# Kernel optimization log

Measured on AMD Instinct MI355X. Metric: run time of the kernel, lower is better.

## Reference

```python
import jax, jax.numpy as jnp
import numpy as np

H = 1024          # hidden_size
NH = 16           # num_attention_heads
HD = H // NH      # attention_head_size = 64
B, S = 8, 1024
LN_EPS = 1e-12


def setup_inputs() -> dict:
    key = jax.random.key(0)
    ks = jax.random.split(key, 12)
    sc = 0.02
    return {
        "input_tensor": jax.random.normal(ks[0], (B, S, H), dtype=jnp.float32),
        "attention_mask": jnp.zeros((B, S), dtype=jnp.float32),
        # LinearMem params (quantization disabled -> plain Linear, torch layout [out,in])
        "Wq": jax.random.normal(ks[1], (H, H), dtype=jnp.float32) * sc,
        "bq": jnp.zeros((H,), dtype=jnp.float32),
        "Wk": jax.random.normal(ks[2], (H, H), dtype=jnp.float32) * sc,
        "bk": jnp.zeros((H,), dtype=jnp.float32),
        "Wv": jax.random.normal(ks[3], (H, H), dtype=jnp.float32) * sc,
        "bv": jnp.zeros((H,), dtype=jnp.float32),
        "Wo": jax.random.normal(ks[4], (H, H), dtype=jnp.float32) * sc,
        "bo": jnp.zeros((H,), dtype=jnp.float32),
        "ln_gamma": jnp.ones((H,), dtype=jnp.float32),
        "ln_beta": jnp.zeros((H,), dtype=jnp.float32),
    }


def _heads(x):  # [B,S,H] -> [B,NH,S,HD]
    return x.reshape(B, S, NH, HD).transpose(0, 2, 1, 3)


def reference(input_tensor, attention_mask, Wq, bq, Wk, bk, Wv, bv, Wo, bo, ln_gamma, ln_beta):
    # Q/K/V projections (LinearMem with quantization disabled == Linear)
    q = _heads(jnp.einsum('bsh,oh->bso', input_tensor, Wq) + bq)
    k = _heads(jnp.einsum('bsh,oh->bso', input_tensor, Wk) + bk)
    v = _heads(jnp.einsum('bsh,oh->bso', input_tensor, Wv) + bv)
    scores = jnp.einsum('bnqd,bnkd->bnqk', q, k) / np.float32(np.sqrt(HD))
    scores = scores + attention_mask[:, None, None, :]  # additive mask [B,1,1,S]
    probs = jax.nn.softmax(scores, axis=-1)  # dropout = identity in eval
    ctx = jnp.einsum('bnqk,bnkd->bnqd', probs, v)
    ctx = ctx.transpose(0, 2, 1, 3).reshape(B, S, H)
    # output projection + residual LayerNorm (eps=1e-12)
    out = jnp.einsum('bsh,oh->bso', ctx, Wo) + bo
    resid = out + input_tensor
    mu = jnp.mean(resid, axis=-1, keepdims=True)
    var = jnp.mean(jnp.square(resid - mu), axis=-1, keepdims=True)
    return (resid - mu) * jax.lax.rsqrt(var + LN_EPS) * ln_gamma + ln_beta
```

## Files before the change

kernel.cpp:

```cpp
#include <hip/hip_runtime.h>

#define NHh 16

typedef unsigned short ushortT;
typedef __attribute__((ext_vector_type(8))) short short8;
typedef __attribute__((ext_vector_type(4))) float floatx4;

__device__ __forceinline__ ushortT f2bf(float x) {
    union { float f; unsigned int u; } cv; cv.f = x;
    unsigned int u = cv.u;
    unsigned int r = u + 0x7fffu + ((u >> 16) & 1u);
    return (ushortT)(r >> 16);
}

__device__ __forceinline__ unsigned pack2_trunc(float a, float b) {
    union { float f; unsigned u; } ua, ub;
    ua.f = a; ub.f = b;
    return (ub.u & 0xffff0000u) | (ua.u >> 16);
}

__device__ __forceinline__ void gload_lds16(const ushortT* g, ushortT* l) {
    __builtin_amdgcn_global_load_lds(
        (const __attribute__((address_space(1))) void*)g,
        (__attribute__((address_space(3))) void*)l, 16, 0, 0);
}

__global__ __launch_bounds__(256) void cvt_x(const float* __restrict__ in,
                                             ushortT* __restrict__ out, int n4) {
    int i = blockIdx.x * 256 + threadIdx.x;
    if (i >= n4) return;
    float4 f = ((const float4*)in)[i];
    uint2 o;
    o.x = (unsigned)f2bf(f.x) | ((unsigned)f2bf(f.y) << 16);
    o.y = (unsigned)f2bf(f.z) | ((unsigned)f2bf(f.w) << 16);
    ((uint2*)out)[i] = o;
}

__global__ __launch_bounds__(256) void cvt_w(const float* __restrict__ W0, const float* __restrict__ W1,
                                             const float* __restrict__ W2, const float* __restrict__ W3,
                                             ushortT* __restrict__ o0, ushortT* __restrict__ o1,
                                             ushortT* __restrict__ o2, ushortT* __restrict__ o3, int n4) {
    int z = blockIdx.y;
    const float* in = (z == 0) ? W0 : (z == 1) ? W1 : (z == 2) ? W2 : W3;
    ushortT* out = (z == 0) ? o0 : (z == 1) ? o1 : (z == 2) ? o2 : o3;
    int i = blockIdx.x * 256 + threadIdx.x;
    if (i >= n4) return;
    float4 f = ((const float4*)in)[i];
    uint2 o;
    o.x = (unsigned)f2bf(f.x) | ((unsigned)f2bf(f.y) << 16);
    o.y = (unsigned)f2bf(f.z) | ((unsigned)f2bf(f.w) << 16);
    ((uint2*)out)[i] = o;
}

__device__ __forceinline__ void gemm_core_256x128(
        const ushortT* __restrict__ Ap, const ushortT* __restrict__ Bp,
        int arow0, int brow0, ushortT* As3, ushortT* Bs3,
        int tid, int wr, int wc, int qd, int ln, floatx4 (&acc)[4][4]) {
    const ushortT* srcA[4]; const ushortT* srcB[2];
    int oA[4], oB[2];
#pragma unroll
    for (int k = 0; k < 4; k++) {
        int o = k * 8192 + tid * 16;
        int rowblk = o >> 11, ks = (o >> 10) & 1, r = (o >> 6) & 15;
        int c2 = ((o >> 4) & 3) ^ ((r >> 3) << 1);
        srcA[k] = Ap + (size_t)(arow0 + rowblk * 16 + r) * 1024 + ks * 32 + c2 * 8;
        oA[k] = o;
    }
#pragma unroll
    for (int k = 0; k < 2; k++) {
        int o = k * 8192 + tid * 16;
        int rowblk = o >> 11, ks = (o >> 10) & 1, r = (o >> 6) & 15;
        int c2 = ((o >> 4) & 3) ^ ((r >> 3) << 1);
        srcB[k] = Bp + (size_t)(brow0 + rowblk * 16 + r) * 1024 + ks * 32 + c2 * 8;
        oB[k] = o;
    }
#pragma unroll
    for (int t = 0; t < 2; t++) {
#pragma unroll
        for (int k = 0; k < 4; k++) {
            gload_lds16(srcA[k], (ushortT*)((char*)As3 + t * 32768 + oA[k]));
            srcA[k] += 64;
        }
#pragma unroll
        for (int k = 0; k < 2; k++) {
            gload_lds16(srcB[k], (ushortT*)((char*)Bs3 + t * 16384 + oB[k]));
            srcB[k] += 64;
        }
    }
    asm volatile("s_waitcnt vmcnt(6)" ::: "memory");
    __builtin_amdgcn_s_barrier();

    const int lnc = ln * 64 + ((qd ^ ((ln >> 3) << 1)) * 16);

    int bi = 0, si = 2;
    for (int T = 0; T < 16; T++) {
        const char* Ab = (const char*)As3 + bi * 32768;
        const char* Bb = (const char*)Bs3 + bi * 16384;
        short8 afr[4][2], bfr[4][2];
#pragma unroll
        for (int mi = 0; mi < 4; mi++)
#pragma unroll
            for (int ks = 0; ks < 2; ks++)
                afr[mi][ks] = *(const short8*)(Ab + (mi * 4 + wr) * 2048 + ks * 1024 + lnc);
#pragma unroll
        for (int ni = 0; ni < 4; ni++)
#pragma unroll
            for (int ks = 0; ks < 2; ks++)
                bfr[ni][ks] = *(const short8*)(Bb + (ni * 2 + wc) * 2048 + ks * 1024 + lnc);
        if (T < 14) {
#pragma unroll
            for (int k = 0; k < 4; k++) {
                gload_lds16(srcA[k], (ushortT*)((char*)As3 + si * 32768 + oA[k]));
                srcA[k] += 64;
            }
#pragma unroll
            for (int k = 0; k < 2; k++) {
                gload_lds16(srcB[k], (ushortT*)((char*)Bs3 + si * 16384 + oB[k]));
                srcB[k] += 64;
            }
        }
        __builtin_amdgcn_s_barrier();
        asm volatile("s_waitcnt lgkmcnt(0)" ::: "memory");
        __builtin_amdgcn_sched_barrier(0);
        __builtin_amdgcn_s_setprio(1);
#pragma unroll
        for (int mi = 0; mi < 4; mi++)
#pragma unroll
            for (int ni = 0; ni < 4; ni++)
#pragma unroll
                for (int ks = 0; ks < 2; ks++)
                    acc[mi][ni] = __builtin_amdgcn_mfma_f32_16x16x32_bf16(
                        afr[mi][ks], bfr[ni][ks], acc[mi][ni], 0, 0, 0);
        __builtin_amdgcn_s_setprio(0);
        if (T < 14) { asm volatile("s_waitcnt vmcnt(6)" ::: "memory"); }
        else        { asm volatile("s_waitcnt vmcnt(0)" ::: "memory"); }
        __builtin_amdgcn_s_barrier();
        bi = (bi == 2) ? 0 : bi + 1;
        si = (si == 2) ? 0 : si + 1;
    }
}

__global__ __launch_bounds__(512, 1) void qkv_gemm3(
        const ushortT* __restrict__ X,
        const ushortT* __restrict__ W0, const ushortT* __restrict__ W1, const ushortT* __restrict__ W2,
        const float* __restrict__ b0, const float* __restrict__ b1, const float* __restrict__ b2,
        ushortT* __restrict__ Qo, ushortT* __restrict__ Ko, ushortT* __restrict__ Vo) {
    __shared__ __align__(16) ushortT As3[3 * 16384];
    __shared__ __align__(16) ushortT Bs3[3 * 8192];

    const int l = blockIdx.x;
    const int xcd = l & 7;
    const int j = l >> 3;
    const int tid = threadIdx.x;
    const int lane = tid & 63;
    const int w = tid >> 6;
    const int wr = w >> 1, wc = w & 1;
    const int qd = lane >> 4, ln = lane & 15;

    int z, arow0, brow0;
    const ushortT* Ap; const ushortT* Bp;
    if (j < 64) {
        z = j >> 5;
        int mg = (j >> 3) & 3;
        int n = j & 7;
        arow0 = (mg * 8 + xcd) * 256;
        brow0 = n * 128;
        Ap = X; Bp = z ? W1 : W0;
    } else {
        z = 2;
        int j2 = j - 64;
        arow0 = (j2 & 3) * 256;
        brow0 = ((j2 >> 2) * 8 + xcd) * 128;
        Ap = W2; Bp = X;
    }

    floatx4 acc[4][4];
#pragma unroll
    for (int i = 0; i < 4; i++)
#pragma unroll
        for (int jj = 0; jj < 4; jj++) acc[i][jj] = (floatx4){0.f, 0.f, 0.f, 0.f};

    gemm_core_256x128(Ap, Bp, arow0, brow0, As3, Bs3, tid, wr, wc, qd, ln, acc);

    if (z == 2) {
        floatx4 bv4[4];
#pragma unroll
        for (int mi = 0; mi < 4; mi++)
            bv4[mi] = *(const floatx4*)(b2 + arow0 + mi * 64 + wr * 16 + qd * 4);
#pragma unroll
        for (int ni = 0; ni < 4; ni++) {
            int n = brow0 + ni * 32 + wc * 16 + ln;
            int bb = n >> 10, s = n & 1023;
#pragma unroll
            for (int mi = 0; mi < 4; mi++) {
#pragma unroll
                for (int r2 = 0; r2 < 4; r2++) {
                    int dim = arow0 + mi * 64 + wr * 16 + qd * 4 + r2;
                    int hh = dim >> 6, dd = dim & 63;
                    Vo[((size_t)(bb * NHh + hh) * 64 + dd) * 1024 + s] =
                        f2bf(acc[mi][ni][r2] + bv4[mi][r2]);
                }
            }
        }
    } else {
        ushortT* Out = z ? Ko : Qo;
        const float* bias = z ? b1 : b0;
#pragma unroll
        for (int ni = 0; ni < 4; ni++) {
            int n = brow0 + ni * 32 + wc * 16 + ln;
            float bb = bias[n];
            int h = n >> 6, d = n & 63;
#pragma unroll
            for (int mi = 0; mi < 4; mi++) {
#pragma unroll
                for (int r2 = 0; r2 < 4; r2++) {
                    int m = arow0 + mi * 64 + wr * 16 + qd * 4 + r2;
                    int b = m >> 10, s = m & 1023;
                    Out[(size_t)((b * NHh + h) * 1024 + s) * 64 + d] =
                        f2bf(acc[mi][ni][r2] + bb);
                }
            }
        }
    }
}

__global__ __launch_bounds__(512, 1) void oproj_gemm3(const ushortT* __restrict__ A,
        const ushortT* __restrict__ Wt, const float* __restrict__ bias, float* __restrict__ Pj) {
    __shared__ __align__(16) ushortT As3[3 * 16384];
    __shared__ __align__(16) ushortT Bs3[3 * 8192];

    const int l = blockIdx.x;
    const int xcd = l & 7;
    const int j = l >> 3;
    const int tid = threadIdx.x;
    const int lane = tid & 63;
    const int w = tid >> 6;
    const int wr = w >> 1, wc = w & 1;
    const int qd = lane >> 4, ln = lane & 15;

    const int arow0 = ((j & 3) * 8 + xcd) * 256;
    const int brow0 = (j >> 2) * 128;

    floatx4 acc[4][4];
#pragma unroll
    for (int i = 0; i < 4; i++)
#pragma unroll
        for (int jj = 0; jj < 4; jj++) acc[i][jj] = (floatx4){0.f, 0.f, 0.f, 0.f};

    gemm_core_256x128(A, Wt, arow0, brow0, As3, Bs3, tid, wr, wc, qd, ln, acc);

#pragma unroll
    for (int ni = 0; ni < 4; ni++) {
        int n = brow0 + ni * 32 + wc * 16 + ln;
        float bb = bias[n];
#pragma unroll
        for (int mi = 0; mi < 4; mi++) {
#pragma unroll
            for (int r2 = 0; r2 < 4; r2++) {
                int m = arow0 + mi * 64 + wr * 16 + qd * 4 + r2;
                Pj[(size_t)m * 1024 + n] = acc[mi][ni][r2] + bb;
            }
        }
    }
}

__global__ __launch_bounds__(256, 2) void attn_kernel(const ushortT* __restrict__ Q,
        const ushortT* __restrict__ K, const ushortT* __restrict__ Vg_t,
        const float* __restrict__ mask, ushortT* __restrict__ ctx) {
    __shared__ __align__(16) ushortT Ks[128 * 64];
    __shared__ __align__(16) ushortT Vt[64 * 128];
    __shared__ __align__(16) ushortT Ps[4][64 * 72];

    const int tid = threadIdx.x;
    const int lane = tid & 63;
    const int w = tid >> 6;
    const int qd = lane >> 4;
    const int ln = lane & 15;
    const int l = blockIdx.x;
    const int bh = l & 127;
    const int b = bh >> 4;
    const int h = bh & 15;
    const int qb = l >> 7;

    const ushortT* Qg = Q + (size_t)bh * 65536;
    const ushortT* Kg = K + (size_t)bh * 65536;
    const ushortT* Vg = Vg_t + (size_t)bh * 65536;
    const float* mrow = mask + b * 1024;
    const float LOG2E = 1.4426950408889634f;
    const float SCL = 0.125f * 1.4426950408889634f;

    short8 qf[4][2];
#pragma unroll
    for (int nj = 0; nj < 4; nj++)
#pragma unroll
        for (int ks = 0; ks < 2; ks++)
            qf[nj][ks] = *(const short8*)(Qg + (size_t)(qb * 256 + w * 64 + nj * 16 + ln) * 64 + ks * 32 + qd * 8);

    float lst[4] = {0.f, 0.f, 0.f, 0.f};
    floatx4 accO[4][4];
#pragma unroll
    for (int i = 0; i < 4; i++)
#pragma unroll
        for (int j = 0; j < 4; j++) accO[i][j] = (floatx4){0.f, 0.f, 0.f, 0.f};

    const int ksr = lane >> 3;
    const int kc  = lane & 7;
    const int vdr = lane >> 4;
    const int vcc = lane & 15;

    for (int kt = 0; kt < 8; ++kt) {
        __syncthreads();

#pragma unroll
        for (int ii = 0; ii < 4; ii++) {
            int i = w * 4 + ii;
            int srow = i * 8 + ksr;
            gload_lds16(Kg + (size_t)(kt * 128 + srow) * 64 + (kc ^ ksr) * 8,
                        Ks + i * 512 + lane * 8);
        }
#pragma unroll
        for (int ii = 0; ii < 4; ii++) {
            int i = w * 4 + ii;
            int d = i * 4 + vdr;
            gload_lds16(Vg + (size_t)d * 1024 + kt * 128 + (vcc ^ (d & 15)) * 8,
                        Vt + i * 512 + lane * 8);
        }

        __syncthreads();

#pragma unroll
        for (int h2 = 0; h2 < 2; ++h2) {
            const int s0g = kt * 128 + h2 * 64;

#pragma unroll
            for (int njp = 0; njp < 2; ++njp) {
                floatx4 sv[4][2];
#pragma unroll
                for (int mi = 0; mi < 4; mi++)
#pragma unroll
                    for (int j = 0; j < 2; j++) sv[mi][j] = (floatx4){0.f, 0.f, 0.f, 0.f};
#pragma unroll
                for (int ks = 0; ks < 2; ks++) {
                    short8 af[4];
#pragma unroll
                    for (int mi = 0; mi < 4; mi++)
                        af[mi] = *(const short8*)&Ks[(h2 * 64 + mi * 16 + ln) * 64 +
                                                     (((ks * 4 + qd) ^ (ln & 7)) * 8)];
#pragma unroll
                    for (int mi = 0; mi < 4; mi++)
#pragma unroll
                        for (int j = 0; j < 2; j++)
                            sv[mi][j] = __builtin_amdgcn_mfma_f32_16x16x32_bf16(af[mi], qf[njp * 2 + j][ks], sv[mi][j], 0, 0, 0);
                }

                float rs0 = 0.f, rs1 = 0.f;
#pragma unroll
                for (int mi = 0; mi < 4; mi++) {
                    floatx4 m4 = *(const floatx4*)(mrow + s0g + mi * 16 + qd * 4);
                    float p00 = __builtin_amdgcn_exp2f(sv[mi][0][0] * SCL + m4[0] * LOG2E);
                    float p01 = __builtin_amdgcn_exp2f(sv[mi][0][1] * SCL + m4[1] * LOG2E);
                    float p02 = __builtin_amdgcn_exp2f(sv[mi][0][2] * SCL + m4[2] * LOG2E);
                    float p03 = __builtin_amdgcn_exp2f(sv[mi][0][3] * SCL + m4[3] * LOG2E);
                    float p10 = __builtin_amdgcn_exp2f(sv[mi][1][0] * SCL + m4[0] * LOG2E);
                    float p11 = __builtin_amdgcn_exp2f(sv[mi][1][1] * SCL + m4[1] * LOG2E);
                    float p12 = __builtin_amdgcn_exp2f(sv[mi][1][2] * SCL + m4[2] * LOG2E);
                    float p13 = __builtin_amdgcn_exp2f(sv[mi][1][3] * SCL + m4[3] * LOG2E);
                    rs0 += (p00 + p01) + (p02 + p03);
                    rs1 += (p10 + p11) + (p12 + p13);
                    uint2 w0, w1;
                    w0.x = pack2_trunc(p00, p01); w0.y = pack2_trunc(p02, p03);
                    w1.x = pack2_trunc(p10, p11); w1.y = pack2_trunc(p12, p13);
                    *(uint2*)&Ps[w][(njp * 32 + ln) * 72 + mi * 16 + qd * 4] = w0;
                    *(uint2*)&Ps[w][(njp * 32 + 16 + ln) * 72 + mi * 16 + qd * 4] = w1;
                }
                rs0 += __shfl_xor(rs0, 16, 64); rs0 += __shfl_xor(rs0, 32, 64);
                rs1 += __shfl_xor(rs1, 16, 64); rs1 += __shfl_xor(rs1, 32, 64);
                lst[njp * 2 + 0] += rs0;
                lst[njp * 2 + 1] += rs1;
            }

#pragma unroll
            for (int ks2 = 0; ks2 < 2; ks2++) {
                short8 ap[4], bv[4];
#pragma unroll
                for (int i = 0; i < 4; i++)
                    ap[i] = *(const short8*)&Ps[w][(i * 16 + ln) * 72 + ks2 * 32 + qd * 8];
#pragma unroll
                for (int j = 0; j < 4; j++)
                    bv[j] = *(const short8*)&Vt[(j * 16 + ln) * 128 +
                                                (((h2 * 8 + ks2 * 4 + qd) ^ ln) * 8)];
#pragma unroll
                for (int i = 0; i < 4; i++)
#pragma unroll
                    for (int j = 0; j < 4; j++)
                        accO[i][j] = __builtin_amdgcn_mfma_f32_16x16x32_bf16(ap[i], bv[j], accO[i][j], 0, 0, 0);
            }
        }
    }

#pragma unroll
    for (int i = 0; i < 4; i++) {
#pragma unroll
        for (int r = 0; r < 4; r++) {
            float lv = __shfl(lst[i], qd * 4 + r, 64);
            float linv = 1.f / lv;
            int q = qb * 256 + w * 64 + i * 16 + qd * 4 + r;
#pragma unroll
            for (int j = 0; j < 4; j++) {
                int d = j * 16 + ln;
                ctx[((size_t)(b * 1024 + q)) * 1024 + h * 64 + d] = f2bf(accO[i][j][r] * linv);
            }
        }
    }
}

__global__ __launch_bounds__(256) void ln_kernel(const float* __restrict__ Pj, const float* __restrict__ X,
        const float* __restrict__ gamma, const float* __restrict__ beta, float* __restrict__ out) {
    __shared__ float red[8];
    int row = blockIdx.x;
    int t = threadIdx.x;
    const float4 p4 = ((const float4*)(Pj + (size_t)row * 1024))[t];
    const float4 x4 = ((const float4*)(X + (size_t)row * 1024))[t];
    float r0 = p4.x + x4.x, r1 = p4.y + x4.y, r2 = p4.z + x4.z, r3 = p4.w + x4.w;
    float s = r0 + r1 + r2 + r3;
    float ss = r0 * r0 + r1 * r1 + r2 * r2 + r3 * r3;
#pragma unroll
    for (int o = 1; o < 64; o <<= 1) { s += __shfl_xor(s, o, 64); ss += __shfl_xor(ss, o, 64); }
    int w = t >> 6;
    if ((t & 63) == 0) { red[w] = s; red[4 + w] = ss; }
    __syncthreads();
    s = red[0] + red[1] + red[2] + red[3];
    ss = red[4] + red[5] + red[6] + red[7];
    float mu = s * (1.f / 1024.f);
    float var = ss * (1.f / 1024.f) - mu * mu;
    float inv = rsqrtf(var + 1e-12f);
    const float4 g4 = ((const float4*)gamma)[t];
    const float4 b4 = ((const float4*)beta)[t];
    float4 o4;
    o4.x = (r0 - mu) * inv * g4.x + b4.x;
    o4.y = (r1 - mu) * inv * g4.y + b4.y;
    o4.z = (r2 - mu) * inv * g4.z + b4.z;
    o4.w = (r3 - mu) * inv * g4.w + b4.w;
    ((float4*)(out + (size_t)row * 1024))[t] = o4;
}

extern "C" void kernel_launch(void* const* d_in, const int* in_sizes, int n_in,
                              void* d_out, int out_size, void* d_ws, size_t ws_size,
                              hipStream_t stream) {
    const float* x     = (const float*)d_in[0];
    const float* mask  = (const float*)d_in[1];
    const float* Wq    = (const float*)d_in[2];
    const float* bq    = (const float*)d_in[3];
    const float* Wk    = (const float*)d_in[4];
    const float* bk    = (const float*)d_in[5];
    const float* Wv    = (const float*)d_in[6];
    const float* bv    = (const float*)d_in[7];
    const float* Wo    = (const float*)d_in[8];
    const float* bo    = (const float*)d_in[9];
    const float* gamma = (const float*)d_in[10];
    const float* beta  = (const float*)d_in[11];
    float* out = (float*)d_out;

    char* ws = (char*)d_ws;
    ushortT* Xb  = (ushortT*)(ws);
    ushortT* Wqb = (ushortT*)(ws + (16u << 20));
    ushortT* Wkb = (ushortT*)(ws + (18u << 20));
    ushortT* Wvb = (ushortT*)(ws + (20u << 20));
    ushortT* Wob = (ushortT*)(ws + (22u << 20));
    ushortT* Qb  = (ushortT*)(ws + (24u << 20));
    ushortT* Kb  = (ushortT*)(ws + (40u << 20));
    ushortT* Vb  = (ushortT*)(ws + (56u << 20));
    ushortT* Cb  = (ushortT*)(ws);
    float*   Pj  = (float*)(ws + (24u << 20));

    cvt_x<<<8192, 256, 0, stream>>>(x, Xb, 2097152);
    cvt_w<<<dim3(1024, 4), 256, 0, stream>>>(Wq, Wk, Wv, Wo, Wqb, Wkb, Wvb, Wob, 262144);
    qkv_gemm3<<<768, 512, 0, stream>>>(Xb, Wqb, Wkb, Wvb, bq, bk, bv, Qb, Kb, Vb);
    attn_kernel<<<512, 256, 0, stream>>>(Qb, Kb, Vb, mask, Cb);
    oproj_gemm3<<<256, 512, 0, stream>>>(Cb, Wob, bo, Pj);
    ln_kernel<<<8192, 256, 0, stream>>>(Pj, x, gamma, beta, out);
}
```

Before: 289.0 us.

## Replace QKV GEMM with fused 256x192 tile kernel over concatenated weights

The Q, K and V weights are now converted into one contiguous [3072,1024] bf16 buffer. A new qkv_st kernel computes 256x192 output tiles over this concatenated N dimension, using 512 blocks instead of 768 and a double-buffered LDS pipeline instead of the triple-buffered shared core. V is no longer computed transposed (W2 x X). It is written from the normal orientation with packed ushort4 stores along the sequence dimension. The aim is fewer, larger tiles with better A reuse. The cost is a shallower prefetch pipeline (vmcnt(0) every iteration), higher register pressure from 24 accumulators per wave, and uneven waves when 512 blocks run on 256 CUs.

```diff
diff --git a/kernel.cpp b/kernel.cpp
--- a/kernel.cpp
+++ b/kernel.cpp
@@ -38,11 +38,10 @@
 
 __global__ __launch_bounds__(256) void cvt_w(const float* __restrict__ W0, const float* __restrict__ W1,
                                              const float* __restrict__ W2, const float* __restrict__ W3,
-                                             ushortT* __restrict__ o0, ushortT* __restrict__ o1,
-                                             ushortT* __restrict__ o2, ushortT* __restrict__ o3, int n4) {
+                                             ushortT* __restrict__ Wall, ushortT* __restrict__ Wob, int n4) {
     int z = blockIdx.y;
     const float* in = (z == 0) ? W0 : (z == 1) ? W1 : (z == 2) ? W2 : W3;
-    ushortT* out = (z == 0) ? o0 : (z == 1) ? o1 : (z == 2) ? o2 : o3;
+    ushortT* out = (z < 3) ? (Wall + (size_t)z * 1048576) : Wob;
     int i = blockIdx.x * 256 + threadIdx.x;
     if (i >= n4) return;
     float4 f = ((const float4*)in)[i];
@@ -50,6 +49,137 @@
     o.x = (unsigned)f2bf(f.x) | ((unsigned)f2bf(f.y) << 16);
     o.y = (unsigned)f2bf(f.z) | ((unsigned)f2bf(f.w) << 16);
     ((uint2*)out)[i] = o;
+}
+
+__global__ __launch_bounds__(512, 1) void qkv_st(
+        const ushortT* __restrict__ X, const ushortT* __restrict__ Wall,
+        const float* __restrict__ b0, const float* __restrict__ b1, const float* __restrict__ b2,
+        ushortT* __restrict__ Qo, ushortT* __restrict__ Ko, ushortT* __restrict__ Vo) {
+    __shared__ __align__(16) ushortT As[2 * 16384];
+    __shared__ __align__(16) ushortT Bs[2 * 12288];
+
+    const int l = blockIdx.x;
+    const int xcd = l & 7;
+    const int j = l >> 3;
+    const int mg = j >> 4;
+    const int nt = j & 15;
+    const int arow0 = (mg * 8 + xcd) * 256;
+    const int brow0 = nt * 192;
+
+    const int tid = threadIdx.x;
+    const int lane = tid & 63;
+    const int w = tid >> 6;
+    const int wr = w >> 2;
+    const int wc = w & 3;
+    const int qd = lane >> 4, ln = lane & 15;
+
+    const ushortT* srcA[4]; const ushortT* srcB[3];
+    int oA[4], oB[3];
+#pragma unroll
+    for (int k = 0; k < 4; k++) {
+        int o = k * 8192 + tid * 16;
+        int rowblk = o >> 11, ks = (o >> 10) & 1, r = (o >> 6) & 15;
+        int c2 = ((o >> 4) & 3) ^ ((r >> 3) << 1);
+        srcA[k] = X + (size_t)(arow0 + rowblk * 16 + r) * 1024 + ks * 32 + c2 * 8;
+        oA[k] = o;
+    }
+#pragma unroll
+    for (int k = 0; k < 3; k++) {
+        int o = k * 8192 + tid * 16;
+        int rowblk = o >> 11, ks = (o >> 10) & 1, r = (o >> 6) & 15;
+        int c2 = ((o >> 4) & 3) ^ ((r >> 3) << 1);
+        srcB[k] = Wall + (size_t)(brow0 + rowblk * 16 + r) * 1024 + ks * 32 + c2 * 8;
+        oB[k] = o;
+    }
+
+    floatx4 acc[8][3];
+#pragma unroll
+    for (int i = 0; i < 8; i++)
+#pragma unroll
+        for (int jj = 0; jj < 3; jj++) acc[i][jj] = (floatx4){0.f, 0.f, 0.f, 0.f};
+
+#pragma unroll
+    for (int k = 0; k < 4; k++) { gload_lds16(srcA[k], As + oA[k] / 2); srcA[k] += 64; }
+#pragma unroll
+    for (int k = 0; k < 3; k++) { gload_lds16(srcB[k], Bs + oB[k] / 2); srcB[k] += 64; }
+    asm volatile("s_waitcnt vmcnt(0)" ::: "memory");
+    __builtin_amdgcn_s_barrier();
+
+    const int lnc = ln * 64 + ((qd ^ ((ln >> 3) << 1)) * 16);
+
+    for (int T = 0; T < 16; T++) {
+        const char* Ab = (const char*)As + (T & 1) * 32768;
+        const char* Bb = (const char*)Bs + (T & 1) * 24576;
+        short8 afr[8][2], bfr[3][2];
+#pragma unroll
+        for (int mi = 0; mi < 8; mi++)
+#pragma unroll
+            for (int ks = 0; ks < 2; ks++)
+                afr[mi][ks] = *(const short8*)(Ab + (wr * 8 + mi) * 2048 + ks * 1024 + lnc);
+#pragma unroll
+        for (int ni = 0; ni < 3; ni++)
+#pragma unroll
+            for (int ks = 0; ks < 2; ks++)
+                bfr[ni][ks] = *(const short8*)(Bb + (wc * 3 + ni) * 2048 + ks * 1024 + lnc);
+        if (T < 15) {
+            char* An = (char*)As + ((T + 1) & 1) * 32768;
+            char* Bn = (char*)Bs + ((T + 1) & 1) * 24576;
+#pragma unroll
+            for (int k = 0; k < 4; k++) { gload_lds16(srcA[k], (ushortT*)(An + oA[k])); srcA[k] += 64; }
+#pragma unroll
+            for (int k = 0; k < 3; k++) { gload_lds16(srcB[k], (ushortT*)(Bn + oB[k])); srcB[k] += 64; }
+        }
+        __builtin_amdgcn_s_barrier();
+        asm volatile("s_waitcnt lgkmcnt(0)" ::: "memory");
+        __builtin_amdgcn_sched_barrier(0);
+        __builtin_amdgcn_s_setprio(1);
+#pragma unroll
+        for (int mi = 0; mi < 8; mi++)
+#pragma unroll
+            for (int ni = 0; ni < 3; ni++)
+#pragma unroll
+                for (int ks = 0; ks < 2; ks++)
+                    acc[mi][ni] = __builtin_amdgcn_mfma_f32_16x16x32_bf16(
+                        afr[mi][ks], bfr[ni][ks], acc[mi][ni], 0, 0, 0);
+        __builtin_amdgcn_s_setprio(0);
+        asm volatile("s_waitcnt vmcnt(0)" ::: "memory");
+        __builtin_amdgcn_s_barrier();
+    }
+
+#pragma unroll
+    for (int ni = 0; ni < 3; ni++) {
+        int n = brow0 + wc * 48 + ni * 16 + ln;
+        int z = n >> 10;
+        int col = n & 1023;
+        int h = col >> 6, d = col & 63;
+        const float* bias = (z == 0) ? b0 : (z == 1) ? b1 : b2;
+        float bb = bias[col];
+        if (z == 2) {
+#pragma unroll
+            for (int mi = 0; mi < 8; mi++) {
+                int m = arow0 + wr * 128 + mi * 16 + qd * 4;
+                int b = m >> 10, s = m & 1023;
+                ushort4 pk;
+                pk.x = f2bf(acc[mi][ni][0] + bb);
+                pk.y = f2bf(acc[mi][ni][1] + bb);
+                pk.z = f2bf(acc[mi][ni][2] + bb);
+                pk.w = f2bf(acc[mi][ni][3] + bb);
+                *(ushort4*)&Vo[((size_t)(b * NHh + h) * 64 + d) * 1024 + s] = pk;
+            }
+        } else {
+            ushortT* Out = z ? Ko : Qo;
+#pragma unroll
+            for (int mi = 0; mi < 8; mi++) {
+#pragma unroll
+                for (int r2 = 0; r2 < 4; r2++) {
+                    int m = arow0 + wr * 128 + mi * 16 + qd * 4 + r2;
+                    int b = m >> 10, s = m & 1023;
+                    Out[(size_t)((b * NHh + h) * 1024 + s) * 64 + d] =
+                        f2bf(acc[mi][ni][r2] + bb);
+                }
+            }
+        }
+    }
 }
 
 __device__ __forceinline__ void gemm_core_256x128(
@@ -137,90 +267,6 @@
         __builtin_amdgcn_s_barrier();
         bi = (bi == 2) ? 0 : bi + 1;
         si = (si == 2) ? 0 : si + 1;
-    }
-}
-
-__global__ __launch_bounds__(512, 1) void qkv_gemm3(
-        const ushortT* __restrict__ X,
-        const ushortT* __restrict__ W0, const ushortT* __restrict__ W1, const ushortT* __restrict__ W2,
-        const float* __restrict__ b0, const float* __restrict__ b1, const float* __restrict__ b2,
-        ushortT* __restrict__ Qo, ushortT* __restrict__ Ko, ushortT* __restrict__ Vo) {
-    __shared__ __align__(16) ushortT As3[3 * 16384];
-    __shared__ __align__(16) ushortT Bs3[3 * 8192];
-
-    const int l = blockIdx.x;
-    const int xcd = l & 7;
-    const int j = l >> 3;
-    const int tid = threadIdx.x;
-    const int lane = tid & 63;
-    const int w = tid >> 6;
-    const int wr = w >> 1, wc = w & 1;
-    const int qd = lane >> 4, ln = lane & 15;
-
-    int z, arow0, brow0;
-    const ushortT* Ap; const ushortT* Bp;
-    if (j < 64) {
-        z = j >> 5;
-        int mg = (j >> 3) & 3;
-        int n = j & 7;
-        arow0 = (mg * 8 + xcd) * 256;
-        brow0 = n * 128;
-        Ap = X; Bp = z ? W1 : W0;
-    } else {
-        z = 2;
-        int j2 = j - 64;
-        arow0 = (j2 & 3) * 256;
-        brow0 = ((j2 >> 2) * 8 + xcd) * 128;
-        Ap = W2; Bp = X;
-    }
-
-    floatx4 acc[4][4];
-#pragma unroll
-    for (int i = 0; i < 4; i++)
-#pragma unroll
-        for (int jj = 0; jj < 4; jj++) acc[i][jj] = (floatx4){0.f, 0.f, 0.f, 0.f};
-
-    gemm_core_256x128(Ap, Bp, arow0, brow0, As3, Bs3, tid, wr, wc, qd, ln, acc);
-
-    if (z == 2) {
-        floatx4 bv4[4];
-#pragma unroll
-        for (int mi = 0; mi < 4; mi++)
-            bv4[mi] = *(const floatx4*)(b2 + arow0 + mi * 64 + wr * 16 + qd * 4);
-#pragma unroll
-        for (int ni = 0; ni < 4; ni++) {
-            int n = brow0 + ni * 32 + wc * 16 + ln;
-            int bb = n >> 10, s = n & 1023;
-#pragma unroll
-            for (int mi = 0; mi < 4; mi++) {
-#pragma unroll
-                for (int r2 = 0; r2 < 4; r2++) {
-                    int dim = arow0 + mi * 64 + wr * 16 + qd * 4 + r2;
-                    int hh = dim >> 6, dd = dim & 63;
-                    Vo[((size_t)(bb * NHh + hh) * 64 + dd) * 1024 + s] =
-                        f2bf(acc[mi][ni][r2] + bv4[mi][r2]);
-                }
-            }
-        }
-    } else {
-        ushortT* Out = z ? Ko : Qo;
-        const float* bias = z ? b1 : b0;
-#pragma unroll
-        for (int ni = 0; ni < 4; ni++) {
-            int n = brow0 + ni * 32 + wc * 16 + ln;
-            float bb = bias[n];
-            int h = n >> 6, d = n & 63;
-#pragma unroll
-            for (int mi = 0; mi < 4; mi++) {
-#pragma unroll
-                for (int r2 = 0; r2 < 4; r2++) {
-                    int m = arow0 + mi * 64 + wr * 16 + qd * 4 + r2;
-                    int b = m >> 10, s = m & 1023;
-                    Out[(size_t)((b * NHh + h) * 1024 + s) * 64 + d] =
-                        f2bf(acc[mi][ni][r2] + bb);
-                }
-            }
-        }
     }
 }
 
@@ -462,20 +508,18 @@
     float* out = (float*)d_out;
 
     char* ws = (char*)d_ws;
-    ushortT* Xb  = (ushortT*)(ws);
-    ushortT* Wqb = (ushortT*)(ws + (16u << 20));
-    ushortT* Wkb = (ushortT*)(ws + (18u << 20));
-    ushortT* Wvb = (ushortT*)(ws + (20u << 20));
-    ushortT* Wob = (ushortT*)(ws + (22u << 20));
-    ushortT* Qb  = (ushortT*)(ws + (24u << 20));
-    ushortT* Kb  = (ushortT*)(ws + (40u << 20));
-    ushortT* Vb  = (ushortT*)(ws + (56u << 20));
-    ushortT* Cb  = (ushortT*)(ws);
-    float*   Pj  = (float*)(ws + (24u << 20));
+    ushortT* Xb   = (ushortT*)(ws);
+    ushortT* Wall = (ushortT*)(ws + (16u << 20));
+    ushortT* Wob  = (ushortT*)(ws + (22u << 20));
+    ushortT* Qb   = (ushortT*)(ws + (24u << 20));
+    ushortT* Kb   = (ushortT*)(ws + (40u << 20));
+    ushortT* Vb   = (ushortT*)(ws + (56u << 20));
+    ushortT* Cb   = (ushortT*)(ws);
+    float*   Pj   = (float*)(ws + (24u << 20));
 
     cvt_x<<<8192, 256, 0, stream>>>(x, Xb, 2097152);
-    cvt_w<<<dim3(1024, 4), 256, 0, stream>>>(Wq, Wk, Wv, Wo, Wqb, Wkb, Wvb, Wob, 262144);
-    qkv_gemm3<<<768, 512, 0, stream>>>(Xb, Wqb, Wkb, Wvb, bq, bk, bv, Qb, Kb, Vb);
+    cvt_w<<<dim3(1024, 4), 256, 0, stream>>>(Wq, Wk, Wv, Wo, Wall, Wob, 262144);
+    qkv_st<<<512, 512, 0, stream>>>(Xb, Wall, bq, bk, bv, Qb, Kb, Vb);
     attn_kernel<<<512, 256, 0, stream>>>(Qb, Kb, Vb, mask, Cb);
     oproj_gemm3<<<256, 512, 0, stream>>>(Cb, Wob, bo, Pj);
     ln_kernel<<<8192, 256, 0, stream>>>(Pj, x, gamma, beta, out);
```

Measured after the change: 276.8 us. 4.2% less time.
